# Performance work log

Hardware: AMD Instinct MI355X
Metric: run time of the kernel (lower is better)

The kernel has to match this reference:

```python
import jax, jax.numpy as jnp
import numpy as np

N, S, C, E = 32768, 32768, 1024, 16384   # nodes, subgraph-node entries, clusters (=B*P), coarsen edges
F, D, B, P, NC = 64, 64, 16, 64, 10      # feat dim, hidden, graphs, patches per graph, classes


def setup_inputs():
    key = jax.random.key(0)
    ks = list(jax.random.split(key, 24))
    p = lambda k, shp: jax.random.normal(k, shp, dtype=jnp.float32) * 0.05
    z = lambda n: jnp.zeros((n,), jnp.float32)
    return {
        "x": jax.random.normal(ks[0], (N, F), dtype=jnp.float32),
        "subgraphs_nodes_mapper": jax.random.randint(ks[1], (S,), 0, N, dtype=jnp.int32),
        "subgraphs_batch": jnp.sort(jax.random.randint(ks[2], (S,), 0, C, dtype=jnp.int32)),
        "subgraphs_batch_row": jax.random.randint(ks[3], (E,), 0, C, dtype=jnp.int32),
        "subgraphs_batch_col": jax.random.randint(ks[4], (E,), 0, C, dtype=jnp.int32),
        "coarsen_edge_attr": jax.random.uniform(ks[5], (E,), dtype=jnp.float32),
        "W_in1": p(ks[6], (F, D)), "b_in1": z(D),
        "W_in2": p(ks[7], (D, D)), "b_in2": z(D),
        "W_pre1": p(ks[8], (D, D)), "b_pre1": z(D),
        "W_pre2": p(ks[9], (D, D)), "b_pre2": z(D),
        "W_post1": p(ks[10], (D, D)), "b_post1": z(D),
        "W_post2": p(ks[11], (D, D)), "b_post2": z(D),
        "W_K": p(ks[12], (D, D)), "b_K": z(D),
        "W_V": p(ks[13], (D, D)), "b_V": z(D),
        "alpha_beta": jax.random.normal(ks[14], (2,), dtype=jnp.float32),
        "W_c1": p(ks[15], (D, D // 2)), "b_c1": z(D // 2),
        "W_c2": p(ks[16], (D // 2, NC)), "b_c2": z(NC),
    }


def reference(x, subgraphs_nodes_mapper, subgraphs_batch, subgraphs_batch_row,
              subgraphs_batch_col, coarsen_edge_attr,
              W_in1, b_in1, W_in2, b_in2, W_pre1, b_pre1, W_pre2, b_pre2,
              W_post1, b_post1, W_post2, b_post2, W_K, b_K, W_V, b_V,
              alpha_beta, W_c1, b_c1, W_c2, b_c2):
    seg_sum = lambda v, idx: jax.ops.segment_sum(v, idx, num_segments=C)
    # input transform MLP (use_gnn=False path)
    h = jax.nn.relu(x @ W_in1 + b_in1)
    h = jax.nn.relu(h @ W_in2 + b_in2)
    sx = h[subgraphs_nodes_mapper]                        # [S, D] irregular gather
    b = subgraphs_batch
    row, col = subgraphs_batch_row, subgraphs_batch_col
    # bincount-based symmetric degree normalization of coarsened edge weights
    deg = seg_sum(coarsen_edge_attr, row)                 # [C]
    dinv = jnp.where(deg > 0, deg ** -0.5, 0.0)
    ea = dinv[row] * coarsen_edge_attr * dinv[col]        # [E]
    # Q path: pre-deepset -> scatter sum -> post-deepset
    Q = jax.nn.relu(sx @ W_pre1 + b_pre1) @ W_pre2 + b_pre2
    Qs = seg_sum(Q, b)
    Qs = jax.nn.relu(Qs @ W_post1 + b_post1) @ W_post2 + b_post2  # [C, D]
    # K / V paths
    K = sx @ W_K + b_K                                    # [S, D]
    cnt = jnp.maximum(seg_sum(jnp.ones((S,), sx.dtype), b), 1.0)
    Ks = seg_sum(K, b) / cnt[:, None]                     # scatter-mean [C, D]
    V = sx @ W_V + b_V                                    # [S, D]
    # relu kernelization
    Qk, Kk, Ksk = jax.nn.relu(Qs), jax.nn.relu(K), jax.nn.relu(Ks)
    ab = jax.nn.softmax(alpha_beta)
    sa, sb = ab[0] ** -0.5, ab[1] ** -0.5
    ck = jnp.concatenate([sa * Ksk[b], sb * Kk], axis=-1)   # [S, 2D]
    cq = jnp.concatenate([sa * Qk, sb * Qk], axis=-1)       # [C, 2D] (diffQ=False)
    ck_s = seg_sum(ck, b)                                   # [C, 2D]
    M = ck[:, :, None] * V[:, None, :]                      # [S, 2D, D] per-entry outer product
    Ms = seg_sum(M, b)                                      # [C, 2D, D]
    # Double_Level_MessageProp / KeyProp on coarsened graph: out[c] = sum_e ea_e * x[row_e] at col_e
    Ms = seg_sum(ea[:, None, None] * Ms[row], col)
    ck_s = seg_sum(ea[:, None] * ck_s[row], col)
    H = jnp.einsum('ci,cij->cj', cq, Ms)                    # [C, D]
    den = jnp.sum(cq * ck_s, axis=-1, keepdims=True) + 1e-6
    out = H / den                                           # [C, D]
    g = out.reshape(B, P, D).mean(axis=1)                   # mean readout over patches
    logits = jax.nn.relu(g @ W_c1 + b_c1) @ W_c2 + b_c2     # [B, NC]
    return logits
```

## Files before the change

kernel.cpp:

```cpp
#include <hip/hip_runtime.h>
#include <math.h>

constexpr int NN = 32768;
constexpr int SS = 32768;
constexpr int CC = 1024;
constexpr int EE = 16384;
constexpr int BB = 16;
constexpr int PP = 64;
constexpr int NC = 10;

__device__ __forceinline__ float rdlane(float v, int l) {
    return __int_as_float(__builtin_amdgcn_readlane(__float_as_int(v), l));
}

#define TS 68

__device__ __forceinline__ void gemm64(const float* A, const float* W,
                                       const float* __restrict__ bias,
                                       int r0, int c0, float acc[4][4])
{
#pragma unroll
    for (int dc = 0; dc < 4; ++dc) {
        float bv = bias[c0 + dc];
        acc[0][dc] = bv; acc[1][dc] = bv; acc[2][dc] = bv; acc[3][dc] = bv;
    }
#pragma unroll 16
    for (int k = 0; k < 64; ++k) {
        float4 av = *(const float4*)(A + k * TS + r0);
        float4 wv = *(const float4*)(W + k * TS + c0);
        acc[0][0] = fmaf(av.x, wv.x, acc[0][0]); acc[0][1] = fmaf(av.x, wv.y, acc[0][1]);
        acc[0][2] = fmaf(av.x, wv.z, acc[0][2]); acc[0][3] = fmaf(av.x, wv.w, acc[0][3]);
        acc[1][0] = fmaf(av.y, wv.x, acc[1][0]); acc[1][1] = fmaf(av.y, wv.y, acc[1][1]);
        acc[1][2] = fmaf(av.y, wv.z, acc[1][2]); acc[1][3] = fmaf(av.y, wv.w, acc[1][3]);
        acc[2][0] = fmaf(av.z, wv.x, acc[2][0]); acc[2][1] = fmaf(av.z, wv.y, acc[2][1]);
        acc[2][2] = fmaf(av.z, wv.z, acc[2][2]); acc[2][3] = fmaf(av.z, wv.w, acc[2][3]);
        acc[3][0] = fmaf(av.w, wv.x, acc[3][0]); acc[3][1] = fmaf(av.w, wv.y, acc[3][1]);
        acc[3][2] = fmaf(av.w, wv.z, acc[3][2]); acc[3][3] = fmaf(av.w, wv.w, acc[3][3]);
    }
}

__device__ __forceinline__ void gemm64x2(const float* A, const float* Wa, const float* Wb,
                                         const float* __restrict__ bias1,
                                         const float* __restrict__ bias2,
                                         int r0, int c0, float acc1[4][4], float acc2[4][4])
{
#pragma unroll
    for (int dc = 0; dc < 4; ++dc) {
        float bv1 = bias1[c0 + dc], bv2 = bias2[c0 + dc];
#pragma unroll
        for (int dr = 0; dr < 4; ++dr) { acc1[dr][dc] = bv1; acc2[dr][dc] = bv2; }
    }
#pragma unroll 8
    for (int k = 0; k < 64; ++k) {
        float4 av = *(const float4*)(A + k * TS + r0);
        float4 w1 = *(const float4*)(Wa + k * TS + c0);
        float4 w2 = *(const float4*)(Wb + k * TS + c0);
        float ar[4] = {av.x, av.y, av.z, av.w};
        float u1[4] = {w1.x, w1.y, w1.z, w1.w};
        float u2[4] = {w2.x, w2.y, w2.z, w2.w};
#pragma unroll
        for (int dr = 0; dr < 4; ++dr)
#pragma unroll
            for (int dc = 0; dc < 4; ++dc) {
                acc1[dr][dc] = fmaf(ar[dr], u1[dc], acc1[dr][dc]);
                acc2[dr][dc] = fmaf(ar[dr], u2[dc], acc2[dr][dc]);
            }
    }
}

__device__ __forceinline__ void writeW(float* dst, int tid,
                                       float4 a, float4 b, float4 c, float4 d)
{
    int colq = (tid & 15) * 4;
    int rb = tid >> 4;
    *(float4*)(dst + (rb     ) * TS + colq) = a;
    *(float4*)(dst + (rb + 16) * TS + colq) = b;
    *(float4*)(dst + (rb + 32) * TS + colq) = c;
    *(float4*)(dst + (rb + 48) * TS + colq) = d;
}

__device__ __forceinline__ void writeXT(float* dst, int tid,
                                        float4 a, float4 b, float4 c, float4 d)
{
    int rb = (tid * 4) & 63;
    int cb = tid >> 4;
    dst[(rb + 0) * TS + cb     ] = a.x;
    dst[(rb + 1) * TS + cb     ] = a.y;
    dst[(rb + 2) * TS + cb     ] = a.z;
    dst[(rb + 3) * TS + cb     ] = a.w;
    dst[(rb + 0) * TS + cb + 16] = b.x;
    dst[(rb + 1) * TS + cb + 16] = b.y;
    dst[(rb + 2) * TS + cb + 16] = b.z;
    dst[(rb + 3) * TS + cb + 16] = b.w;
    dst[(rb + 0) * TS + cb + 32] = c.x;
    dst[(rb + 1) * TS + cb + 32] = c.y;
    dst[(rb + 2) * TS + cb + 32] = c.z;
    dst[(rb + 3) * TS + cb + 32] = c.w;
    dst[(rb + 0) * TS + cb + 48] = d.x;
    dst[(rb + 1) * TS + cb + 48] = d.y;
    dst[(rb + 2) * TS + cb + 48] = d.z;
    dst[(rb + 3) * TS + cb + 48] = d.w;
}

__device__ __forceinline__ void outT_relu(float* dst, int r0, int c0, float acc[4][4])
{
#pragma unroll
    for (int dc = 0; dc < 4; ++dc) {
        *(float4*)(dst + (c0 + dc) * TS + r0) =
            make_float4(fmaxf(acc[0][dc], 0.f), fmaxf(acc[1][dc], 0.f),
                        fmaxf(acc[2][dc], 0.f), fmaxf(acc[3][dc], 0.f));
    }
}

__device__ __forceinline__ void outG2(float* __restrict__ dst, size_t rowbase, int ld,
                                      int off, int r0, int c0, float acc[4][4], bool dorelu)
{
#pragma unroll
    for (int dr = 0; dr < 4; ++dr) {
        float4 v = make_float4(acc[dr][0], acc[dr][1], acc[dr][2], acc[dr][3]);
        if (dorelu) {
            v.x = fmaxf(v.x, 0.f); v.y = fmaxf(v.y, 0.f);
            v.z = fmaxf(v.z, 0.f); v.w = fmaxf(v.w, 0.f);
        }
        *(float4*)(dst + (rowbase + r0 + dr) * ld + off + c0) = v;
    }
}

__global__ __launch_bounds__(256, 2) void k_node(
    const float* __restrict__ x,
    const int* __restrict__ row, const float* __restrict__ attr,
    const int* __restrict__ batch,
    const float* __restrict__ W1, const float* __restrict__ b1,
    const float* __restrict__ W2, const float* __restrict__ b2,
    const float* __restrict__ Wp1, const float* __restrict__ bp1,
    const float* __restrict__ WK, const float* __restrict__ bK,
    const float* __restrict__ WV, const float* __restrict__ bV,
    float* __restrict__ u, float* __restrict__ KV,
    float* __restrict__ deg, int* __restrict__ segoff, float* __restrict__ zbase)
{
    __shared__ __align__(16) float bufA[64 * TS];
    __shared__ __align__(16) float bufB[64 * TS];
    __shared__ __align__(16) float w0[64 * TS];
    __shared__ __align__(16) float w1[64 * TS];
    __shared__ float ldeg[16];
    int tid = threadIdx.x;
    int b = blockIdx.x;
    if (tid < 33) {
        int i = b * 33 + tid;
        if (i < 16640) ((float4*)zbase)[i] = make_float4(0.f, 0.f, 0.f, 0.f);
    }
    if (b < 64) {
        if (tid < 16) ldeg[tid] = 0.f;
        __syncthreads();
        int lo = b * 16;
#pragma unroll 4
        for (int i = 0; i < 64; ++i) {
            int e = i * 256 + tid;
            int r = row[e];
            unsigned d = (unsigned)(r - lo);
            if (d < 16u) atomicAdd(&ldeg[d], attr[e]);
        }
        __syncthreads();
        if (tid < 16) deg[lo + tid] = ldeg[tid];
    } else if (b < 192) {
        int t = (b - 64) * 256 + tid;
        int cur = batch[t];
        int prev = (t == 0) ? -1 : batch[t - 1];
        for (int c = prev + 1; c <= cur; ++c) segoff[c] = t;
        if (t == SS - 1)
            for (int c = cur + 1; c <= CC; ++c) segoff[c] = SS;
    }
    int tx = tid & 15, ty = tid >> 4;
    int r0 = ty * 4, c0 = tx * 4;
    size_t rowbase = (size_t)b * 64;
    const float* xb = x + rowbase * 64;
    float4 a0 = ((const float4*)W1)[tid];
    float4 a1 = ((const float4*)W1)[tid + 256];
    float4 a2 = ((const float4*)W1)[tid + 512];
    float4 a3 = ((const float4*)W1)[tid + 768];
    float4 x0 = ((const float4*)xb)[tid];
    float4 x1 = ((const float4*)xb)[tid + 256];
    float4 x2 = ((const float4*)xb)[tid + 512];
    float4 x3 = ((const float4*)xb)[tid + 768];
    writeW(w0, tid, a0, a1, a2, a3);
    writeXT(bufA, tid, x0, x1, x2, x3);
    __syncthreads();
    float acc[4][4], accV[4][4];
    a0 = ((const float4*)W2)[tid];
    a1 = ((const float4*)W2)[tid + 256];
    a2 = ((const float4*)W2)[tid + 512];
    a3 = ((const float4*)W2)[tid + 768];
    gemm64(bufA, w0, b1, r0, c0, acc);
    outT_relu(bufB, r0, c0, acc);
    writeW(w1, tid, a0, a1, a2, a3);
    __syncthreads();
    a0 = ((const float4*)Wp1)[tid];
    a1 = ((const float4*)Wp1)[tid + 256];
    a2 = ((const float4*)Wp1)[tid + 512];
    a3 = ((const float4*)Wp1)[tid + 768];
    gemm64(bufB, w1, b2, r0, c0, acc);
    outT_relu(bufA, r0, c0, acc);
    writeW(w0, tid, a0, a1, a2, a3);
    __syncthreads();
    a0 = ((const float4*)WK)[tid];
    a1 = ((const float4*)WK)[tid + 256];
    a2 = ((const float4*)WK)[tid + 512];
    a3 = ((const float4*)WK)[tid + 768];
    float4 v0 = ((const float4*)WV)[tid];
    float4 v1 = ((const float4*)WV)[tid + 256];
    float4 v2 = ((const float4*)WV)[tid + 512];
    float4 v3 = ((const float4*)WV)[tid + 768];
    gemm64(bufA, w0, bp1, r0, c0, acc);
    outG2(u, rowbase, 64, 0, r0, c0, acc, true);
    writeW(w1, tid, a0, a1, a2, a3);
    writeW(bufB, tid, v0, v1, v2, v3);
    __syncthreads();
    gemm64x2(bufA, w1, bufB, bK, bV, r0, c0, acc, accV);
    outG2(KV, rowbase, 128, 0, r0, c0, acc, false);
    outG2(KV, rowbase, 128, 64, r0, c0, accV, false);
}

__global__ __launch_bounds__(256, 4) void k_qk(
    const float* __restrict__ u, const int* __restrict__ mapper,
    const int* __restrict__ segoff,
    const float* __restrict__ Wp2, const float* __restrict__ bp2,
    const float* __restrict__ Wpo1, const float* __restrict__ bpo1,
    const float* __restrict__ Wpo2, const float* __restrict__ bpo2,
    float* __restrict__ Qk)
{
    __shared__ float accs[4][64];
    int c = blockIdx.x;
    int tid = threadIdx.x, j = tid & 63, g = tid >> 6;
    int s0 = segoff[c], s1 = segoff[c + 1];
    float L = (float)(s1 - s0);
    if (tid < 64) {
        accs[0][tid] = 0.f;
        accs[1][tid] = L * bp2[tid];
        accs[2][tid] = bpo1[tid];
        accs[3][tid] = bpo2[tid];
    }
    __syncthreads();
    float us = 0.f;
    for (int s = s0 + g; s < s1; s += 4) us += u[(size_t)mapper[s] * 64 + j];
    atomicAdd(&accs[0][j], us);
    __syncthreads();
    float usv = accs[0][j];
    float p = 0.f;
#pragma unroll
    for (int t = 0; t < 16; ++t) {
        int i = g * 16 + t;
        p = fmaf(rdlane(usv, i), Wp2[i * 64 + j], p);
    }
    atomicAdd(&accs[1][j], p);
    __syncthreads();
    float qs = accs[1][j];
    p = 0.f;
#pragma unroll
    for (int t = 0; t < 16; ++t) {
        int i = g * 16 + t;
        p = fmaf(rdlane(qs, i), Wpo1[i * 64 + j], p);
    }
    atomicAdd(&accs[2][j], p);
    __syncthreads();
    float tv = fmaxf(accs[2][j], 0.f);
    p = 0.f;
#pragma unroll
    for (int t = 0; t < 16; ++t) {
        int i = g * 16 + t;
        p = fmaf(rdlane(tv, i), Wpo2[i * 64 + j], p);
    }
    atomicAdd(&accs[3][j], p);
    __syncthreads();
    if (g == 0) Qk[c * 64 + j] = fmaxf(accs[3][j], 0.f);
}

#define KSTR 72
#define MSTR 68

__global__ __launch_bounds__(256, 4) void k_msbedge(
    const float* __restrict__ KV, const int* __restrict__ mapper,
    const int* __restrict__ segoff, const float* __restrict__ Qk,
    const int* __restrict__ row, const int* __restrict__ col,
    const float* __restrict__ attr, const float* __restrict__ deg,
    const float* __restrict__ ab,
    float* __restrict__ H, float* __restrict__ den)
{
    __shared__ __align__(16) float Kr[32 * KSTR];
    __shared__ __align__(16) float Vb[32 * KSTR];
    __shared__ __align__(16) float msb[64 * MSTR];
    __shared__ int map_lds[32];
    __shared__ float sums[192];
    __shared__ int eids[128];
    __shared__ int ecnt;
    int c = blockIdx.x;
    int tid = threadIdx.x, j = tid & 63, g = tid >> 6;
    int tx = tid & 15, ty = tid >> 4;
    int r0 = ty * 4, c0 = tx * 4;
    if (tid == 0) ecnt = 0;
    if (tid < 192) sums[tid] = 0.f;
    __syncthreads();
#pragma unroll 4
    for (int i = 0; i < 64; ++i) {
        int e = i * 256 + tid;
        if (row[e] == c) {
            int p = atomicAdd(&ecnt, 1);
            if (p < 128) eids[p] = e;
        }
    }
    __syncthreads();
    int ne = min(ecnt, 128);
    if (ne == 0) return;
    int s0 = segoff[c], s1 = segoff[c + 1];
    float acc[4][4];
#pragma unroll
    for (int a = 0; a < 4; ++a)
#pragma unroll
        for (int bq = 0; bq < 4; ++bq) acc[a][bq] = 0.f;
    float ks = 0.f, krs = 0.f, vs = 0.f;
    for (int sb = s0; sb < s1; sb += 32) {
        int clen = min(32, s1 - sb);
        __syncthreads();
        if (tid < clen) map_lds[tid] = mapper[sb + tid];
        __syncthreads();
        for (int p = tid; p < clen * 32; p += 256) {
            int e = p >> 5, q = p & 31;
            int m = map_lds[e];
            float4 v = *(const float4*)(KV + (size_t)m * 128 + q * 4);
            float* dst = (q < 16) ? &Kr[e * KSTR + q * 4] : &Vb[e * KSTR + (q - 16) * 4];
            *(float4*)dst = v;
        }
        __syncthreads();
#pragma unroll 4
        for (int s = 0; s < clen; ++s) {
            float4 a4 = *(const float4*)(&Kr[s * KSTR + r0]);
            float4 b4 = *(const float4*)(&Vb[s * KSTR + c0]);
            float ar0 = fmaxf(a4.x, 0.f), ar1 = fmaxf(a4.y, 0.f);
            float ar2 = fmaxf(a4.z, 0.f), ar3 = fmaxf(a4.w, 0.f);
            acc[0][0] = fmaf(ar0, b4.x, acc[0][0]); acc[0][1] = fmaf(ar0, b4.y, acc[0][1]);
            acc[0][2] = fmaf(ar0, b4.z, acc[0][2]); acc[0][3] = fmaf(ar0, b4.w, acc[0][3]);
            acc[1][0] = fmaf(ar1, b4.x, acc[1][0]); acc[1][1] = fmaf(ar1, b4.y, acc[1][1]);
            acc[1][2] = fmaf(ar1, b4.z, acc[1][2]); acc[1][3] = fmaf(ar1, b4.w, acc[1][3]);
            acc[2][0] = fmaf(ar2, b4.x, acc[2][0]); acc[2][1] = fmaf(ar2, b4.y, acc[2][1]);
            acc[2][2] = fmaf(ar2, b4.z, acc[2][2]); acc[2][3] = fmaf(ar2, b4.w, acc[2][3]);
            acc[3][0] = fmaf(ar3, b4.x, acc[3][0]); acc[3][1] = fmaf(ar3, b4.y, acc[3][1]);
            acc[3][2] = fmaf(ar3, b4.z, acc[3][2]); acc[3][3] = fmaf(ar3, b4.w, acc[3][3]);
        }
        for (int s = g; s < clen; s += 4) {
            float kv = Kr[s * KSTR + j];
            ks += kv;
            krs += fmaxf(kv, 0.f);
            vs += Vb[s * KSTR + j];
        }
    }
#pragma unroll
    for (int a = 0; a < 4; ++a)
        *(float4*)(&msb[(r0 + a) * MSTR + c0]) =
            make_float4(acc[a][0], acc[a][1], acc[a][2], acc[a][3]);
    atomicAdd(&sums[j], ks);
    atomicAdd(&sums[64 + j], krs);
    atomicAdd(&sums[128 + j], vs);
    __syncthreads();
    int L = s1 - s0;
    float Lr = (float)L;
    float Lm = (float)(L > 0 ? L : 1);
    float kskj = fmaxf(sums[j] / Lm, 0.f);
    float krj  = sums[64 + j];
    float vsj  = sums[128 + j];
    float dr   = deg[c];
    float dinvr = dr > 0.f ? 1.f / sqrtf(dr) : 0.f;
    float a0 = ab[0], a1 = ab[1];
    float sa2 = 1.f + expf(a1 - a0);
    float sb2 = 1.f + expf(a0 - a1);
    int idx = g;
    if (idx >= ne) return;
    int e = eids[idx];
    int cdst = col[e];
    float at = attr[e];
    float dc = deg[cdst];
    float qv = Qk[cdst * 64 + j];
    while (true) {
        int cc = cdst; float atc = at, dcc = dc, qc = qv;
        int nidx = idx + 4;
        if (nidx < ne) {
            int e2 = eids[nidx];
            cdst = col[e2];
            at = attr[e2];
            dc = deg[cdst];
            qv = Qk[cdst * 64 + j];
        }
        float dinvc = dcc > 0.f ? 1.f / sqrtf(dcc) : 0.f;
        float wc = dinvr * atc * dinvc;
        float wj0 = 0.f, wj1 = 0.f, wj2 = 0.f, wj3 = 0.f;
#pragma unroll
        for (int t = 0; t < 16; ++t) {
            wj0 = fmaf(rdlane(qc, 4 * t + 0), msb[(4 * t + 0) * MSTR + j], wj0);
            wj1 = fmaf(rdlane(qc, 4 * t + 1), msb[(4 * t + 1) * MSTR + j], wj1);
            wj2 = fmaf(rdlane(qc, 4 * t + 2), msb[(4 * t + 2) * MSTR + j], wj2);
            wj3 = fmaf(rdlane(qc, 4 * t + 3), msb[(4 * t + 3) * MSTR + j], wj3);
        }
        float wjt = (wj0 + wj1) + (wj2 + wj3);
        float p1 = qc * kskj;
        float p2 = qc * krj;
#pragma unroll
        for (int o = 32; o > 0; o >>= 1) { p1 += __shfl_xor(p1, o); p2 += __shfl_xor(p2, o); }
        atomicAdd(&H[cc * 64 + j], wc * (sb2 * wjt + sa2 * p1 * vsj));
        if (j == 0) atomicAdd(&den[cc], wc * (sa2 * Lr * p1 + sb2 * p2));
        idx = nidx;
        if (idx >= ne) break;
    }
}

__global__ __launch_bounds__(64) void k_final(
    const float* __restrict__ H, const float* __restrict__ den,
    const float* __restrict__ Wc1, const float* __restrict__ bc1,
    const float* __restrict__ Wc2, const float* __restrict__ bc2,
    float* __restrict__ out)
{
    int bg = blockIdx.x;
    int j = threadIdx.x;
    float acc = 0.f;
    for (int p = 0; p < PP; ++p) {
        int c = bg * PP + p;
        acc += H[c * 64 + j] / (den[c] + 1e-6f);
    }
    float g = acc * (1.f / (float)PP);
    int m = j & 31;
    float a1 = bc1[m];
#pragma unroll
    for (int i = 0; i < 64; ++i) a1 = fmaf(rdlane(g, i), Wc1[i * 32 + m], a1);
    float c1 = fmaxf(a1, 0.f);
    int n = (j < NC) ? j : 0;
    float a2 = bc2[n];
#pragma unroll
    for (int i = 0; i < 32; ++i) a2 = fmaf(rdlane(c1, i), Wc2[i * NC + n], a2);
    if (j < NC) out[bg * NC + j] = a2;
}

extern "C" void kernel_launch(void* const* d_in, const int* in_sizes, int n_in,
                              void* d_out, int out_size, void* d_ws, size_t ws_size,
                              hipStream_t stream)
{
    const float* x      = (const float*)d_in[0];
    const int*   mapper = (const int*)d_in[1];
    const int*   batch  = (const int*)d_in[2];
    const int*   row    = (const int*)d_in[3];
    const int*   col    = (const int*)d_in[4];
    const float* attr   = (const float*)d_in[5];
    const float* W_in1  = (const float*)d_in[6];
    const float* b_in1  = (const float*)d_in[7];
    const float* W_in2  = (const float*)d_in[8];
    const float* b_in2  = (const float*)d_in[9];
    const float* W_pre1 = (const float*)d_in[10];
    const float* b_pre1 = (const float*)d_in[11];
    const float* W_pre2 = (const float*)d_in[12];
    const float* b_pre2 = (const float*)d_in[13];
    const float* W_post1= (const float*)d_in[14];
    const float* b_post1= (const float*)d_in[15];
    const float* W_post2= (const float*)d_in[16];
    const float* b_post2= (const float*)d_in[17];
    const float* W_K    = (const float*)d_in[18];
    const float* b_K    = (const float*)d_in[19];
    const float* W_V    = (const float*)d_in[20];
    const float* b_V    = (const float*)d_in[21];
    const float* alpha_beta = (const float*)d_in[22];
    const float* W_c1   = (const float*)d_in[23];
    const float* b_c1   = (const float*)d_in[24];
    const float* W_c2   = (const float*)d_in[25];
    const float* b_c2   = (const float*)d_in[26];

    float* ws = (float*)d_ws;
    float* u     = ws;
    float* KV    = u     + (size_t)NN * 64;
    float* Qk    = KV    + (size_t)NN * 128;
    float* deg   = Qk    + (size_t)CC * 64;
    float* H     = deg   + (size_t)CC;
    float* den   = H     + (size_t)CC * 64;
    int*  segoff = (int*)(den + (size_t)CC);

    k_node<<<NN / 64, 256, 0, stream>>>(x, row, attr, batch,
                                        W_in1, b_in1, W_in2, b_in2,
                                        W_pre1, b_pre1, W_K, b_K, W_V, b_V,
                                        u, KV, deg, segoff, H);
    k_qk<<<CC, 256, 0, stream>>>(u, mapper, segoff, W_pre2, b_pre2,
                                 W_post1, b_post1, W_post2, b_post2, Qk);
    k_msbedge<<<CC, 256, 0, stream>>>(KV, mapper, segoff, Qk, row, col,
                                      attr, deg, alpha_beta, H, den);
    k_final<<<BB, 64, 0, stream>>>(H, den, W_c1, b_c1, W_c2, b_c2, (float*)d_out);
}
```

Measured before the change: 89.03 us.

## Fold rank-1 terms into msb and batch edge processing through LDS

The K/V GEMM is merged with the Wp1 GEMM into one three-output pass, which removes a barrier and a round trip through shared memory. In k_msbedge the rank-1 correction terms (ksk⊗vs and the denominator vector) are folded into the msb matrix and a dvec before the edge loop, so each edge needs only a q·M product. Edges are processed 16 at a time, with their Q rows staged in LDS and float4 tiled accumulation. The chunk size for the K/V staging is halved to 16, trading extra loop iterations and barriers for lower LDS use.

```diff
diff --git a/kernel.cpp b/kernel.cpp
--- a/kernel.cpp
+++ b/kernel.cpp
@@ -39,31 +39,37 @@
     }
 }
 
-__device__ __forceinline__ void gemm64x2(const float* A, const float* Wa, const float* Wb,
-                                         const float* __restrict__ bias1,
-                                         const float* __restrict__ bias2,
-                                         int r0, int c0, float acc1[4][4], float acc2[4][4])
+__device__ __forceinline__ void gemm64x3(const float* A, const float* Wa,
+                                         const float* Wb, const float* Wc_,
+                                         const float* __restrict__ b1_,
+                                         const float* __restrict__ b2_,
+                                         const float* __restrict__ b3_,
+                                         int r0, int c0,
+                                         float a1_[4][4], float a2_[4][4], float a3_[4][4])
 {
 #pragma unroll
     for (int dc = 0; dc < 4; ++dc) {
-        float bv1 = bias1[c0 + dc], bv2 = bias2[c0 + dc];
-#pragma unroll
-        for (int dr = 0; dr < 4; ++dr) { acc1[dr][dc] = bv1; acc2[dr][dc] = bv2; }
-    }
-#pragma unroll 8
+        float v1 = b1_[c0 + dc], v2 = b2_[c0 + dc], v3 = b3_[c0 + dc];
+#pragma unroll
+        for (int dr = 0; dr < 4; ++dr) { a1_[dr][dc] = v1; a2_[dr][dc] = v2; a3_[dr][dc] = v3; }
+    }
+#pragma unroll 4
     for (int k = 0; k < 64; ++k) {
         float4 av = *(const float4*)(A + k * TS + r0);
         float4 w1 = *(const float4*)(Wa + k * TS + c0);
         float4 w2 = *(const float4*)(Wb + k * TS + c0);
+        float4 w3 = *(const float4*)(Wc_ + k * TS + c0);
         float ar[4] = {av.x, av.y, av.z, av.w};
         float u1[4] = {w1.x, w1.y, w1.z, w1.w};
         float u2[4] = {w2.x, w2.y, w2.z, w2.w};
+        float u3[4] = {w3.x, w3.y, w3.z, w3.w};
 #pragma unroll
         for (int dr = 0; dr < 4; ++dr)
 #pragma unroll
             for (int dc = 0; dc < 4; ++dc) {
-                acc1[dr][dc] = fmaf(ar[dr], u1[dc], acc1[dr][dc]);
-                acc2[dr][dc] = fmaf(ar[dr], u2[dc], acc2[dr][dc]);
+                a1_[dr][dc] = fmaf(ar[dr], u1[dc], a1_[dr][dc]);
+                a2_[dr][dc] = fmaf(ar[dr], u2[dc], a2_[dr][dc]);
+                a3_[dr][dc] = fmaf(ar[dr], u3[dc], a3_[dr][dc]);
             }
     }
 }
@@ -185,7 +191,7 @@
     writeW(w0, tid, a0, a1, a2, a3);
     writeXT(bufA, tid, x0, x1, x2, x3);
     __syncthreads();
-    float acc[4][4], accV[4][4];
+    float acc[4][4];
     a0 = ((const float4*)W2)[tid];
     a1 = ((const float4*)W2)[tid + 256];
     a2 = ((const float4*)W2)[tid + 512];
@@ -198,25 +204,24 @@
     a1 = ((const float4*)Wp1)[tid + 256];
     a2 = ((const float4*)Wp1)[tid + 512];
     a3 = ((const float4*)Wp1)[tid + 768];
-    gemm64(bufB, w1, b2, r0, c0, acc);
-    outT_relu(bufA, r0, c0, acc);
-    writeW(w0, tid, a0, a1, a2, a3);
-    __syncthreads();
-    a0 = ((const float4*)WK)[tid];
-    a1 = ((const float4*)WK)[tid + 256];
-    a2 = ((const float4*)WK)[tid + 512];
-    a3 = ((const float4*)WK)[tid + 768];
+    float4 k0 = ((const float4*)WK)[tid];
+    float4 k1 = ((const float4*)WK)[tid + 256];
+    float4 k2 = ((const float4*)WK)[tid + 512];
+    float4 k3 = ((const float4*)WK)[tid + 768];
     float4 v0 = ((const float4*)WV)[tid];
     float4 v1 = ((const float4*)WV)[tid + 256];
     float4 v2 = ((const float4*)WV)[tid + 512];
     float4 v3 = ((const float4*)WV)[tid + 768];
-    gemm64(bufA, w0, bp1, r0, c0, acc);
-    outG2(u, rowbase, 64, 0, r0, c0, acc, true);
-    writeW(w1, tid, a0, a1, a2, a3);
+    gemm64(bufB, w1, b2, r0, c0, acc);
+    outT_relu(bufA, r0, c0, acc);
+    writeW(w0, tid, a0, a1, a2, a3);
+    writeW(w1, tid, k0, k1, k2, k3);
     writeW(bufB, tid, v0, v1, v2, v3);
     __syncthreads();
-    gemm64x2(bufA, w1, bufB, bK, bV, r0, c0, acc, accV);
-    outG2(KV, rowbase, 128, 0, r0, c0, acc, false);
+    float accU[4][4], accK[4][4], accV[4][4];
+    gemm64x3(bufA, w0, w1, bufB, bp1, bK, bV, r0, c0, accU, accK, accV);
+    outG2(u, rowbase, 64, 0, r0, c0, accU, true);
+    outG2(KV, rowbase, 128, 0, r0, c0, accK, false);
     outG2(KV, rowbase, 128, 64, r0, c0, accV, false);
 }
 
@@ -276,6 +281,7 @@
 
 #define KSTR 72
 #define MSTR 68
+#define QSTR 68
 
 __global__ __launch_bounds__(256, 4) void k_msbedge(
     const float* __restrict__ KV, const int* __restrict__ mapper,
@@ -285,17 +291,20 @@
     const float* __restrict__ ab,
     float* __restrict__ H, float* __restrict__ den)
 {
-    __shared__ __align__(16) float Kr[32 * KSTR];
-    __shared__ __align__(16) float Vb[32 * KSTR];
+    __shared__ __align__(16) float Kr[16 * KSTR];
+    __shared__ __align__(16) float Vb[16 * KSTR];
     __shared__ __align__(16) float msb[64 * MSTR];
-    __shared__ int map_lds[32];
+    __shared__ __align__(16) float qlds[16 * QSTR];
+    __shared__ int map_lds[16];
     __shared__ float sums[192];
+    __shared__ float dvec[64];
     __shared__ int eids[128];
     __shared__ int ecnt;
     int c = blockIdx.x;
-    int tid = threadIdx.x, j = tid & 63, g = tid >> 6;
+    int tid = threadIdx.x, j = tid & 63;
     int tx = tid & 15, ty = tid >> 4;
     int r0 = ty * 4, c0 = tx * 4;
+    int g = tid >> 6;
     if (tid == 0) ecnt = 0;
     if (tid < 192) sums[tid] = 0.f;
     __syncthreads();
@@ -317,8 +326,8 @@
 #pragma unroll
         for (int bq = 0; bq < 4; ++bq) acc[a][bq] = 0.f;
     float ks = 0.f, krs = 0.f, vs = 0.f;
-    for (int sb = s0; sb < s1; sb += 32) {
-        int clen = min(32, s1 - sb);
+    for (int sb = s0; sb < s1; sb += 16) {
+        int clen = min(16, s1 - sb);
         __syncthreads();
         if (tid < clen) map_lds[tid] = mapper[sb + tid];
         __syncthreads();
@@ -352,61 +361,77 @@
             vs += Vb[s * KSTR + j];
         }
     }
-#pragma unroll
-    for (int a = 0; a < 4; ++a)
-        *(float4*)(&msb[(r0 + a) * MSTR + c0]) =
-            make_float4(acc[a][0], acc[a][1], acc[a][2], acc[a][3]);
     atomicAdd(&sums[j], ks);
     atomicAdd(&sums[64 + j], krs);
     atomicAdd(&sums[128 + j], vs);
     __syncthreads();
     int L = s1 - s0;
     float Lr = (float)L;
-    float Lm = (float)(L > 0 ? L : 1);
-    float kskj = fmaxf(sums[j] / Lm, 0.f);
-    float krj  = sums[64 + j];
-    float vsj  = sums[128 + j];
-    float dr   = deg[c];
-    float dinvr = dr > 0.f ? 1.f / sqrtf(dr) : 0.f;
+    float invLm = 1.f / (float)(L > 0 ? L : 1);
     float a0 = ab[0], a1 = ab[1];
     float sa2 = 1.f + expf(a1 - a0);
     float sb2 = 1.f + expf(a0 - a1);
-    int idx = g;
-    if (idx >= ne) return;
-    int e = eids[idx];
-    int cdst = col[e];
-    float at = attr[e];
-    float dc = deg[cdst];
-    float qv = Qk[cdst * 64 + j];
-    while (true) {
-        int cc = cdst; float atc = at, dcc = dc, qc = qv;
-        int nidx = idx + 4;
-        if (nidx < ne) {
-            int e2 = eids[nidx];
-            cdst = col[e2];
-            at = attr[e2];
-            dc = deg[cdst];
-            qv = Qk[cdst * 64 + j];
-        }
-        float dinvc = dcc > 0.f ? 1.f / sqrtf(dcc) : 0.f;
-        float wc = dinvr * atc * dinvc;
-        float wj0 = 0.f, wj1 = 0.f, wj2 = 0.f, wj3 = 0.f;
-#pragma unroll
-        for (int t = 0; t < 16; ++t) {
-            wj0 = fmaf(rdlane(qc, 4 * t + 0), msb[(4 * t + 0) * MSTR + j], wj0);
-            wj1 = fmaf(rdlane(qc, 4 * t + 1), msb[(4 * t + 1) * MSTR + j], wj1);
-            wj2 = fmaf(rdlane(qc, 4 * t + 2), msb[(4 * t + 2) * MSTR + j], wj2);
-            wj3 = fmaf(rdlane(qc, 4 * t + 3), msb[(4 * t + 3) * MSTR + j], wj3);
-        }
-        float wjt = (wj0 + wj1) + (wj2 + wj3);
-        float p1 = qc * kskj;
-        float p2 = qc * krj;
-#pragma unroll
-        for (int o = 32; o > 0; o >>= 1) { p1 += __shfl_xor(p1, o); p2 += __shfl_xor(p2, o); }
-        atomicAdd(&H[cc * 64 + j], wc * (sb2 * wjt + sa2 * p1 * vsj));
-        if (j == 0) atomicAdd(&den[cc], wc * (sa2 * Lr * p1 + sb2 * p2));
-        idx = nidx;
-        if (idx >= ne) break;
+    if (tid < 64) {
+        float kskv = fmaxf(sums[tid] * invLm, 0.f);
+        dvec[tid] = sa2 * Lr * kskv + sb2 * sums[64 + tid];
+    }
+    float4 vsl4 = *(const float4*)(&sums[128 + c0]);
+#pragma unroll
+    for (int a = 0; a < 4; ++a) {
+        float kska = fmaxf(sums[r0 + a] * invLm, 0.f) * sa2;
+        *(float4*)(&msb[(r0 + a) * MSTR + c0]) =
+            make_float4(fmaf(kska, vsl4.x, sb2 * acc[a][0]),
+                        fmaf(kska, vsl4.y, sb2 * acc[a][1]),
+                        fmaf(kska, vsl4.z, sb2 * acc[a][2]),
+                        fmaf(kska, vsl4.w, sb2 * acc[a][3]));
+    }
+    float dr = deg[c];
+    float dinvr = dr > 0.f ? 1.f / sqrtf(dr) : 0.f;
+    __syncthreads();
+    float dvreg = dvec[j];
+    int te = tid >> 4, tc = tid & 15;
+    for (int base = 0; base < ne; base += 16) {
+        if (base) __syncthreads();
+        int mye = base + te;
+        bool act = mye < ne;
+        int cdst = 0; float wt = 0.f;
+        if (act) {
+            int e = eids[mye];
+            cdst = col[e];
+            *(float4*)(&qlds[te * QSTR + tc * 4]) =
+                *(const float4*)(Qk + (size_t)cdst * 64 + tc * 4);
+            float dc = deg[cdst];
+            float dinvc = dc > 0.f ? 1.f / sqrtf(dc) : 0.f;
+            wt = dinvr * attr[e] * dinvc;
+        }
+        __syncthreads();
+        float pd[4];
+#pragma unroll
+        for (int t = 0; t < 4; ++t) {
+            float q = qlds[(g * 4 + t) * QSTR + j];
+            float pv = q * dvreg;
+#pragma unroll
+            for (int o = 32; o > 0; o >>= 1) pv += __shfl_xor(pv, o);
+            pd[t] = pv;
+        }
+        float pdsel = pd[te & 3];
+        if (act) {
+            float o0 = 0.f, o1 = 0.f, o2 = 0.f, o3 = 0.f;
+            const float* qrow = &qlds[te * QSTR];
+#pragma unroll 8
+            for (int k = 0; k < 64; ++k) {
+                float q = qrow[k];
+                float4 m4 = *(const float4*)(&msb[k * MSTR + tc * 4]);
+                o0 = fmaf(q, m4.x, o0); o1 = fmaf(q, m4.y, o1);
+                o2 = fmaf(q, m4.z, o2); o3 = fmaf(q, m4.w, o3);
+            }
+            float* hdst = &H[(size_t)cdst * 64 + tc * 4];
+            atomicAdd(hdst + 0, wt * o0);
+            atomicAdd(hdst + 1, wt * o1);
+            atomicAdd(hdst + 2, wt * o2);
+            atomicAdd(hdst + 3, wt * o3);
+            if (tc == 0) atomicAdd(&den[cdst], wt * pdsel);
+        }
     }
 }
 
```

After: 96.01 us. +7.8%, slower.

## Fold rank-one terms into msb, batch four edges per wave, shrink k_node LDS

Applied to the files above, without the earlier changes.

In k_node, the second weight buffer is removed so the LDS footprint allows three blocks per CU. The pre1 and K GEMMs are now fused, followed by a separate V GEMM, which adds extra barriers. In k_msbedge, the rank-one mean-key times value-sum term is folded algebraically into the msb matrix, and the denominator vector is precomputed once. The edge weights and destination columns are staged in LDS, and each wave processes four edges per iteration so one msb read is reused across four dot products. This reduces per-edge LDS traffic and readlane overhead, and padding edges with zero weight adds a few wasted atomics.

```diff
diff --git a/kernel.cpp b/kernel.cpp
--- a/kernel.cpp
+++ b/kernel.cpp
@@ -126,7 +126,7 @@
     }
 }
 
-__global__ __launch_bounds__(256, 2) void k_node(
+__global__ __launch_bounds__(256, 3) void k_node(
     const float* __restrict__ x,
     const int* __restrict__ row, const float* __restrict__ attr,
     const int* __restrict__ batch,
@@ -141,7 +141,6 @@
     __shared__ __align__(16) float bufA[64 * TS];
     __shared__ __align__(16) float bufB[64 * TS];
     __shared__ __align__(16) float w0[64 * TS];
-    __shared__ __align__(16) float w1[64 * TS];
     __shared__ float ldeg[16];
     int tid = threadIdx.x;
     int b = blockIdx.x;
@@ -185,39 +184,42 @@
     writeW(w0, tid, a0, a1, a2, a3);
     writeXT(bufA, tid, x0, x1, x2, x3);
     __syncthreads();
-    float acc[4][4], accV[4][4];
+    float acc[4][4], acc2[4][4];
     a0 = ((const float4*)W2)[tid];
     a1 = ((const float4*)W2)[tid + 256];
     a2 = ((const float4*)W2)[tid + 512];
     a3 = ((const float4*)W2)[tid + 768];
     gemm64(bufA, w0, b1, r0, c0, acc);
     outT_relu(bufB, r0, c0, acc);
-    writeW(w1, tid, a0, a1, a2, a3);
+    __syncthreads();
+    writeW(w0, tid, a0, a1, a2, a3);
     __syncthreads();
     a0 = ((const float4*)Wp1)[tid];
     a1 = ((const float4*)Wp1)[tid + 256];
     a2 = ((const float4*)Wp1)[tid + 512];
     a3 = ((const float4*)Wp1)[tid + 768];
-    gemm64(bufB, w1, b2, r0, c0, acc);
+    float4 k0 = ((const float4*)WK)[tid];
+    float4 k1 = ((const float4*)WK)[tid + 256];
+    float4 k2 = ((const float4*)WK)[tid + 512];
+    float4 k3 = ((const float4*)WK)[tid + 768];
+    gemm64(bufB, w0, b2, r0, c0, acc);
     outT_relu(bufA, r0, c0, acc);
+    __syncthreads();
     writeW(w0, tid, a0, a1, a2, a3);
-    __syncthreads();
-    a0 = ((const float4*)WK)[tid];
-    a1 = ((const float4*)WK)[tid + 256];
-    a2 = ((const float4*)WK)[tid + 512];
-    a3 = ((const float4*)WK)[tid + 768];
-    float4 v0 = ((const float4*)WV)[tid];
-    float4 v1 = ((const float4*)WV)[tid + 256];
-    float4 v2 = ((const float4*)WV)[tid + 512];
-    float4 v3 = ((const float4*)WV)[tid + 768];
-    gemm64(bufA, w0, bp1, r0, c0, acc);
+    writeW(bufB, tid, k0, k1, k2, k3);
+    __syncthreads();
+    a0 = ((const float4*)WV)[tid];
+    a1 = ((const float4*)WV)[tid + 256];
+    a2 = ((const float4*)WV)[tid + 512];
+    a3 = ((const float4*)WV)[tid + 768];
+    gemm64x2(bufA, w0, bufB, bp1, bK, r0, c0, acc, acc2);
     outG2(u, rowbase, 64, 0, r0, c0, acc, true);
-    writeW(w1, tid, a0, a1, a2, a3);
-    writeW(bufB, tid, v0, v1, v2, v3);
-    __syncthreads();
-    gemm64x2(bufA, w1, bufB, bK, bV, r0, c0, acc, accV);
-    outG2(KV, rowbase, 128, 0, r0, c0, acc, false);
-    outG2(KV, rowbase, 128, 64, r0, c0, accV, false);
+    outG2(KV, rowbase, 128, 0, r0, c0, acc2, false);
+    __syncthreads();
+    writeW(w0, tid, a0, a1, a2, a3);
+    __syncthreads();
+    gemm64(bufA, w0, bV, r0, c0, acc);
+    outG2(KV, rowbase, 128, 64, r0, c0, acc, false);
 }
 
 __global__ __launch_bounds__(256, 4) void k_qk(
@@ -290,7 +292,10 @@
     __shared__ __align__(16) float msb[64 * MSTR];
     __shared__ int map_lds[32];
     __shared__ float sums[192];
+    __shared__ float dvec[64];
     __shared__ int eids[128];
+    __shared__ int ecol[144];
+    __shared__ float ewt[144];
     __shared__ int ecnt;
     int c = blockIdx.x;
     int tid = threadIdx.x, j = tid & 63, g = tid >> 6;
@@ -352,61 +357,80 @@
             vs += Vb[s * KSTR + j];
         }
     }
-#pragma unroll
-    for (int a = 0; a < 4; ++a)
-        *(float4*)(&msb[(r0 + a) * MSTR + c0]) =
-            make_float4(acc[a][0], acc[a][1], acc[a][2], acc[a][3]);
     atomicAdd(&sums[j], ks);
     atomicAdd(&sums[64 + j], krs);
     atomicAdd(&sums[128 + j], vs);
     __syncthreads();
     int L = s1 - s0;
     float Lr = (float)L;
-    float Lm = (float)(L > 0 ? L : 1);
-    float kskj = fmaxf(sums[j] / Lm, 0.f);
-    float krj  = sums[64 + j];
-    float vsj  = sums[128 + j];
-    float dr   = deg[c];
-    float dinvr = dr > 0.f ? 1.f / sqrtf(dr) : 0.f;
+    float invLm = 1.f / (float)(L > 0 ? L : 1);
     float a0 = ab[0], a1 = ab[1];
     float sa2 = 1.f + expf(a1 - a0);
     float sb2 = 1.f + expf(a0 - a1);
-    int idx = g;
-    if (idx >= ne) return;
-    int e = eids[idx];
-    int cdst = col[e];
-    float at = attr[e];
-    float dc = deg[cdst];
-    float qv = Qk[cdst * 64 + j];
-    while (true) {
-        int cc = cdst; float atc = at, dcc = dc, qc = qv;
-        int nidx = idx + 4;
-        if (nidx < ne) {
-            int e2 = eids[nidx];
-            cdst = col[e2];
-            at = attr[e2];
-            dc = deg[cdst];
-            qv = Qk[cdst * 64 + j];
-        }
-        float dinvc = dcc > 0.f ? 1.f / sqrtf(dcc) : 0.f;
-        float wc = dinvr * atc * dinvc;
-        float wj0 = 0.f, wj1 = 0.f, wj2 = 0.f, wj3 = 0.f;
-#pragma unroll
-        for (int t = 0; t < 16; ++t) {
-            wj0 = fmaf(rdlane(qc, 4 * t + 0), msb[(4 * t + 0) * MSTR + j], wj0);
-            wj1 = fmaf(rdlane(qc, 4 * t + 1), msb[(4 * t + 1) * MSTR + j], wj1);
-            wj2 = fmaf(rdlane(qc, 4 * t + 2), msb[(4 * t + 2) * MSTR + j], wj2);
-            wj3 = fmaf(rdlane(qc, 4 * t + 3), msb[(4 * t + 3) * MSTR + j], wj3);
-        }
-        float wjt = (wj0 + wj1) + (wj2 + wj3);
-        float p1 = qc * kskj;
-        float p2 = qc * krj;
-#pragma unroll
-        for (int o = 32; o > 0; o >>= 1) { p1 += __shfl_xor(p1, o); p2 += __shfl_xor(p2, o); }
-        atomicAdd(&H[cc * 64 + j], wc * (sb2 * wjt + sa2 * p1 * vsj));
-        if (j == 0) atomicAdd(&den[cc], wc * (sa2 * Lr * p1 + sb2 * p2));
-        idx = nidx;
-        if (idx >= ne) break;
+    float dr = deg[c];
+    float dinvr = dr > 0.f ? 1.f / sqrtf(dr) : 0.f;
+    if (tid < 64) {
+        float kskv = fmaxf(sums[tid] * invLm, 0.f);
+        dvec[tid] = sa2 * Lr * kskv + sb2 * sums[64 + tid];
+    }
+    float4 vsl4 = *(const float4*)(&sums[128 + c0]);
+#pragma unroll
+    for (int a = 0; a < 4; ++a) {
+        float kska = fmaxf(sums[r0 + a] * invLm, 0.f) * sa2;
+        *(float4*)(&msb[(r0 + a) * MSTR + c0]) =
+            make_float4(fmaf(kska, vsl4.x, sb2 * acc[a][0]),
+                        fmaf(kska, vsl4.y, sb2 * acc[a][1]),
+                        fmaf(kska, vsl4.z, sb2 * acc[a][2]),
+                        fmaf(kska, vsl4.w, sb2 * acc[a][3]));
+    }
+    int nr = (ne + 15) & ~15;
+    if (tid < ne) {
+        int e = eids[tid];
+        int cd = col[e];
+        float dc = deg[cd];
+        float dinvc = dc > 0.f ? 1.f / sqrtf(dc) : 0.f;
+        ecol[tid] = cd;
+        ewt[tid] = dinvr * attr[e] * dinvc;
+    }
+    for (int p = ne + tid; p < nr; p += 256) { ecol[p] = c; ewt[p] = 0.f; }
+    __syncthreads();
+    float dvreg = dvec[j];
+    for (int m0 = g * 4; m0 < nr; m0 += 16) {
+        int cd0 = ecol[m0 + 0], cd1 = ecol[m0 + 1];
+        int cd2 = ecol[m0 + 2], cd3 = ecol[m0 + 3];
+        float wt0 = ewt[m0 + 0], wt1 = ewt[m0 + 1];
+        float wt2 = ewt[m0 + 2], wt3 = ewt[m0 + 3];
+        float q0 = Qk[(size_t)cd0 * 64 + j];
+        float q1 = Qk[(size_t)cd1 * 64 + j];
+        float q2 = Qk[(size_t)cd2 * 64 + j];
+        float q3 = Qk[(size_t)cd3 * 64 + j];
+        float o0 = 0.f, o1 = 0.f, o2 = 0.f, o3 = 0.f;
+#pragma unroll
+        for (int i = 0; i < 64; ++i) {
+            float mv = msb[i * MSTR + j];
+            o0 = fmaf(rdlane(q0, i), mv, o0);
+            o1 = fmaf(rdlane(q1, i), mv, o1);
+            o2 = fmaf(rdlane(q2, i), mv, o2);
+            o3 = fmaf(rdlane(q3, i), mv, o3);
+        }
+        float p0 = q0 * dvreg, p1 = q1 * dvreg, p2 = q2 * dvreg, p3 = q3 * dvreg;
+#pragma unroll
+        for (int o = 32; o > 0; o >>= 1) {
+            p0 += __shfl_xor(p0, o);
+            p1 += __shfl_xor(p1, o);
+            p2 += __shfl_xor(p2, o);
+            p3 += __shfl_xor(p3, o);
+        }
+        atomicAdd(&H[(size_t)cd0 * 64 + j], wt0 * o0);
+        atomicAdd(&H[(size_t)cd1 * 64 + j], wt1 * o1);
+        atomicAdd(&H[(size_t)cd2 * 64 + j], wt2 * o2);
+        atomicAdd(&H[(size_t)cd3 * 64 + j], wt3 * o3);
+        if (j == 0) {
+            atomicAdd(&den[cd0], wt0 * p0);
+            atomicAdd(&den[cd1], wt1 * p1);
+            atomicAdd(&den[cd2], wt2 * p2);
+            atomicAdd(&den[cd3], wt3 * p3);
+        }
     }
 }
 
```

Result: slower. 94.71 us (+6.4%).
